# Kernel tuning notes

Measured on AMD Instinct MI355X. Metric: run time of the kernel, lower is better.

Reference implementation:

```python
import jax, jax.numpy as jnp
import numpy as np

B, N, D, H, L, F = 8192, 64, 128, 8, 3, 512
HD = D // H
RADIUS = 3.0
LN_EPS = 1e-5


def _ln(x, g, b):
    m = jnp.mean(x, axis=-1, keepdims=True)
    v = jnp.var(x, axis=-1, keepdims=True)
    return (x - m) / jnp.sqrt(v + LN_EPS) * g + b


def setup_inputs() -> dict:
    key = jax.random.key(0)
    ks = jax.random.split(key, 20)
    def nrm(k, shape, s=0.05):
        return jax.random.normal(k, shape, jnp.float32) * s
    return {
        'ego_context': nrm(ks[0], (B, D), 1.0),
        'ego_pos': nrm(ks[1], (B, 2), 1.0),
        'ego_vel': nrm(ks[2], (B, 2), 1.0),
        'neighbor_pos': nrm(ks[3], (B, N, 2), 1.5),
        'neighbor_vel': nrm(ks[4], (B, N, 2), 1.0),
        'neighbor_mask': jax.random.bernoulli(ks[5], 0.8, (B, N)),
        'np_W': nrm(ks[6], (6, D), 0.3), 'np_b': jnp.zeros((D,), jnp.float32),
        'np_ln_g': jnp.ones((D,), jnp.float32), 'np_ln_b': jnp.zeros((D,), jnp.float32),
        'ego_W': nrm(ks[7], (D, D)), 'ego_b': jnp.zeros((D,), jnp.float32),
        'ego_ln_g': jnp.ones((D,), jnp.float32), 'ego_ln_b': jnp.zeros((D,), jnp.float32),
        'n1_g': jnp.ones((L, D), jnp.float32), 'n1_b': jnp.zeros((L, D), jnp.float32),
        'nkv_g': jnp.ones((L, D), jnp.float32), 'nkv_b': jnp.zeros((L, D), jnp.float32),
        'n2_g': jnp.ones((L, D), jnp.float32), 'n2_b': jnp.zeros((L, D), jnp.float32),
        'Wq': nrm(ks[8], (L, D, D)), 'bq': jnp.zeros((L, D), jnp.float32),
        'Wk': nrm(ks[9], (L, D, D)), 'bk': jnp.zeros((L, D), jnp.float32),
        'Wv': nrm(ks[10], (L, D, D)), 'bv': jnp.zeros((L, D), jnp.float32),
        'Wo': nrm(ks[11], (L, D, D)), 'bo': jnp.zeros((L, D), jnp.float32),
        'W1': nrm(ks[12], (L, D, F)), 'b1': jnp.zeros((L, F), jnp.float32),
        'W2': nrm(ks[13], (L, F, D)), 'b2': jnp.zeros((L, D), jnp.float32),
        'out_W': nrm(ks[14], (D, D)), 'out_b': jnp.zeros((D,), jnp.float32),
        'out_ln_g': jnp.ones((D,), jnp.float32), 'out_ln_b': jnp.zeros((D,), jnp.float32),
    }


def reference(ego_context, ego_pos, ego_vel, neighbor_pos, neighbor_vel, neighbor_mask,
              np_W, np_b, np_ln_g, np_ln_b, ego_W, ego_b, ego_ln_g, ego_ln_b,
              n1_g, n1_b, nkv_g, nkv_b, n2_g, n2_b,
              Wq, bq, Wk, bk, Wv, bv, Wo, bo, W1, b1, W2, b2,
              out_W, out_b, out_ln_g, out_ln_b):
    # relative features (B, N, 6)
    rel_pos = neighbor_pos - ego_pos[:, None, :]
    rel_vel = neighbor_vel - ego_vel[:, None, :]
    dist = jnp.clip(jnp.linalg.norm(rel_pos, axis=-1, keepdims=True), 1e-6, None)
    bearing = jnp.arctan2(rel_pos[..., 1:2] + 1e-8, rel_pos[..., 0:1] + 1e-8)
    rel = jnp.concatenate([rel_pos, rel_vel, dist, bearing], axis=-1)

    # dynamic mask: radius gating + all-masked fixup (mimics key_padding_mask[all_masked,0]=False)
    valid = neighbor_mask & (jnp.linalg.norm(neighbor_pos - ego_pos[:, None, :], axis=-1) < RADIUS)
    all_invalid = ~jnp.any(valid, axis=-1)
    valid = valid | (all_invalid[:, None] & (jnp.arange(N) == 0)[None, :])

    # neighbor_proj: Linear(6,D) -> LN -> ReLU (dropout inactive at eval)
    nb = jax.nn.relu(_ln(rel @ np_W + np_b, np_ln_g, np_ln_b))  # (B, N, D)
    # ego_proj: Linear(D,D) -> LN; keep ego as (B, D) since query length is 1
    x = _ln(ego_context @ ego_W + ego_b, ego_ln_g, ego_ln_b)

    scale = 1.0 / jnp.sqrt(jnp.float32(HD))
    for i in range(L):
        q = _ln(x, n1_g[i], n1_b[i])          # (B, D)
        kv = _ln(nb, nkv_g[i], nkv_b[i])      # (B, N, D)
        Q = (q @ Wq[i] + bq[i]).reshape(B, H, HD)
        K = (kv @ Wk[i] + bk[i]).reshape(B, N, H, HD)
        V = (kv @ Wv[i] + bv[i]).reshape(B, N, H, HD)
        scores = jnp.einsum('bhd,bnhd->bhn', Q, K) * scale
        scores = jnp.where(valid[:, None, :], scores, -1e9)
        attn = jax.nn.softmax(scores, axis=-1)
        ctx = jnp.einsum('bhn,bnhd->bhd', attn, V).reshape(B, D)
        x = x + ctx @ Wo[i] + bo[i]
        y = _ln(x, n2_g[i], n2_b[i])
        x = x + jax.nn.gelu(y @ W1[i] + b1[i], approximate=False) @ W2[i] + b2[i]

    return _ln(x @ out_W + out_b, out_ln_g, out_ln_b)
```

## Files before the change

kernel.cpp:

```cpp
#include <hip/hip_runtime.h>
#include <stdint.h>

typedef unsigned int uint;
typedef unsigned short ushort;
typedef unsigned long long u64;

#define B_   8192
#define D_   128
#define N_   64
#define L_   3

typedef __attribute__((ext_vector_type(8))) short short8;
typedef __attribute__((ext_vector_type(4))) float f32x4;
union FragU { uint4 u; short8 h; };

__device__ __forceinline__ float bf2f(ushort u){ union{uint i; float f;} c; c.i=((uint)u)<<16; return c.f; }
__device__ __forceinline__ float bflo(uint u){ union{uint i; float f;} c; c.i=u<<16; return c.f; }
__device__ __forceinline__ float bfhi(uint u){ union{uint i; float f;} c; c.i=u&0xffff0000u; return c.f; }
__device__ __forceinline__ ushort f2bf(float f){ uint u=__float_as_uint(f); return (ushort)((u + 0x7fffu + ((u>>16)&1u))>>16); }
__device__ __forceinline__ uint pk2(float lo, float hi){ return (uint)f2bf(lo) | (((uint)f2bf(hi))<<16); }
__device__ __forceinline__ float wsum(float v){ for (int o=32;o;o>>=1) v += __shfl_xor(v,o); return v; }

__device__ ushort g_WqT[3*128*128];
__device__ ushort g_WkT[3*128*128];
__device__ ushort g_WvT[3*128*128];
__device__ ushort g_WoT[3*128*128];
__device__ ushort g_W1T[3*512*128];
__device__ ushort g_W2T[3*128*512];
__device__ ushort g_egoT[128*128];
__device__ ushort g_outT[128*128];
__device__ float  g_npRec[128*9];
__device__ ushort g_bqF[384];
__device__ ushort g_bkF[384];
__device__ ushort g_bvF[384];
__device__ ushort g_b1F[1536];
__device__ u64    g_msk[B_];

#define OFF_X   0
#define XSTR    520
#define OFF_XH  8320
#define XHSTR   272
#define OFF_Q   12672
#define QSTR    260
#define OFF_QK  16832
#define QKSTR   272
#define OFF_QB  21184
#define OFF_V   21248
#define OFF_NB  21504
#define NBSTR   272
#define OFF_NT  38912
#define NTSTR   144
#define OFF_AT  57344
#define ATSTR   144
#define OFF_U   59648
#define OFF_CX  61760
#define OFF_H1  21504
#define LDS_SZ  62272

struct P {
  const float *ego, *epos, *evel, *npos, *nvel;
  const int   *mask;
  const float *npW, *npb, *npg, *npbb;
  const float *ego_b, *ego_g, *ego_bb;
  const float *bo, *b2, *out_b, *out_g, *out_bb;
  ushort *nbg;
  float *outp;
};

template<int MODE>
__global__ __launch_bounds__(256,4) void prep_all(P p,
    const float* Wq,const float* bq,const float* n1g,const float* n1b,
    const float* Wk,const float* bk,const float* nkg,const float* nkb,
    const float* Wv,const float* bv,
    const float* W1,const float* b1,const float* n2g,const float* n2b,
    const float* Wo,const float* W2,const float* egoW,const float* outW){
  __shared__ float red[2];
  __shared__ float s_npW[768], s_npP[384];
  __shared__ float s_valid[2][64];
  __shared__ __align__(16) ushort s_T[2][128][68];
  const int bid = blockIdx.x;
  const int tid = threadIdx.x;
  if (bid < 2688){
    int t = tid;
    const float *src,*g,*bb,*bias; ushort *dstW,*dstB; int N;
    if (bid<384){ int l=bid>>7, j=bid&127; src=Wq+l*16384+j; g=n1g+l*128; bb=n1b+l*128; bias=bq+l*128+j; dstW=g_WqT+l*16384+j*128; dstB=g_bqF+l*128+j; N=128; }
    else if (bid<768){ int q=bid-384; int l=q>>7, j=q&127; src=Wk+l*16384+j; g=nkg+l*128; bb=nkb+l*128; bias=bk+l*128+j; dstW=g_WkT+l*16384+j*128; dstB=g_bkF+l*128+j; N=128; }
    else if (bid<1152){ int q=bid-768; int l=q>>7, j=q&127; src=Wv+l*16384+j; g=nkg+l*128; bb=nkb+l*128; bias=bv+l*128+j; dstW=g_WvT+l*16384+j*128; dstB=g_bvF+l*128+j; N=128; }
    else { int q=bid-1152; int l=q/512, j=q%512; src=W1+l*65536+j; g=n2g+l*128; bb=n2b+l*128; bias=b1+l*512+j; dstW=g_W1T+l*65536+j*128; dstB=g_b1F+l*512+j; N=512; }
    if (t<128){
      float wv = src[t*N];
      dstW[t] = f2bf(g[t]*wv);
      float pv = wsum(bb[t]*wv);
      if ((t&63)==0) red[t>>6]=pv;
    }
    __syncthreads();
    if (t==0) *dstB = f2bf(red[0]+red[1]+bias[0]);
  } else if (bid < 3712){
    int pb = bid - 2688, t = tid;
    if (t<128){
      if (pb<384){ int l=pb>>7, j=pb&127; g_WoT[l*16384+j*128+t] = f2bf(Wo[l*16384+t*128+j]); }
      else if (pb<768){ int q=pb-384; int l=q>>7, j=q&127;
        for (int k=t;k<512;k+=128) g_W2T[l*65536+j*512+k] = f2bf(W2[l*65536+k*128+j]); }
      else if (pb<896){ int j=pb-768; g_egoT[j*128+t]=f2bf(egoW[t*128+j]); }
      else { int j=pb-896; g_outT[j*128+t]=f2bf(outW[t*128+j]); }
    }
  } else if (bid == 3712){
    int t = tid;
    if (t<128){
      for (int r=0;r<6;++r) g_npRec[t*9+r]=p.npW[r*128+t];
      g_npRec[t*9+6]=p.npb[t]; g_npRec[t*9+7]=p.npg[t]; g_npRec[t*9+8]=p.npbb[t];
    }
  } else {
    const int bq2 = bid - 3713;
    const int g = tid>>7, t = tid&127;
    const int b = bq2*2+g;
    for (int i=tid;i<768;i+=256) s_npW[i]=p.npW[i];
    if (tid<128){ s_npP[tid]=p.npb[tid]; s_npP[128+tid]=p.npg[tid]; s_npP[256+tid]=p.npbb[tid]; }
    __syncthreads();
    int nn=t>>1, jh=t&1;
    float2 pn = ((const float2*)p.npos)[b*N_+nn];
    float2 vn = ((const float2*)p.nvel)[b*N_+nn];
    float2 pe = ((const float2*)p.epos)[b];
    float2 ve = ((const float2*)p.evel)[b];
    float rx=pn.x-pe.x, ry=pn.y-pe.y, rvx=vn.x-ve.x, rvy=vn.y-ve.y;
    float nrm = sqrtf(rx*rx+ry*ry);
    float dist = fmaxf(nrm,1e-6f), bear = atan2f(ry+1e-8f, rx+1e-8f);
    bool vld = (p.mask[b*N_+nn]!=0) && (nrm<3.0f);
    if (jh==0) s_valid[g][nn] = vld?1.f:0.f;
    float z[64]; float sa=0.f, sb=0.f;
    #pragma unroll
    for (int jj=0;jj<64;++jj){
      int j = jh*64+jj;
      float v = s_npP[j] + rx*s_npW[j] + ry*s_npW[128+j] + rvx*s_npW[256+j]
                         + rvy*s_npW[384+j] + dist*s_npW[512+j] + bear*s_npW[640+j];
      z[jj]=v; sa+=v; sb+=v*v;
    }
    sa += __shfl_xor(sa,1); sb += __shfl_xor(sb,1);
    float m1 = sa*0.0078125f, r1 = rsqrtf(sb*0.0078125f - m1*m1 + 1e-5f);
    float ta=0.f, tb=0.f;
    #pragma unroll
    for (int jj=0;jj<64;++jj){
      int j = jh*64+jj;
      float a = (z[jj]-m1)*r1*s_npP[128+j] + s_npP[256+j];
      a = fmaxf(a,0.f);
      z[jj]=a; ta+=a; tb+=a*a;
    }
    ta += __shfl_xor(ta,1); tb += __shfl_xor(tb,1);
    float m2 = ta*0.0078125f, r2 = rsqrtf(tb*0.0078125f - m2*m2 + 1e-5f);
    uint4* dst4 = (uint4*)((char*)p.nbg + (size_t)b*32768 + (size_t)t*128);
    #pragma unroll
    for (int q8=0;q8<8;++q8){
      uint prs[4];
      #pragma unroll
      for (int qi=0;qi<4;++qi){
        int q = q8*4+qi;
        uint pr = pk2((z[2*q]-m2)*r2, (z[2*q+1]-m2)*r2);
        prs[qi]=pr;
        int d = jh*64 + 2*q;
        s_T[g][d][nn]   = (ushort)pr;
        s_T[g][d+1][nn] = (ushort)(pr>>16);
      }
      uint4 ov; ov.x=prs[0]; ov.y=prs[1]; ov.z=prs[2]; ov.w=prs[3];
      dst4[q8] = ov;
    }
    __syncthreads();
    const int b0 = bq2*2;
    #pragma unroll
    for (int i=0;i<8;++i){
      int idx = tid + i*256;
      int g2 = idx>>10, k = idx&1023;
      int d = k>>3, n0 = (k&7)*8;
      const ushort* srcT = &s_T[g2][d][n0];
      uint2 v0 = *(const uint2*)srcT;
      uint2 v1 = *(const uint2*)(srcT+4);
      uint4 outv; outv.x=v0.x; outv.y=v0.y; outv.z=v1.x; outv.w=v1.y;
      *(uint4*)((char*)p.nbg + (size_t)(b0+g2)*32768 + 16384 + (size_t)k*16) = outv;
    }
    if (tid<2){
      u64 m=0;
      for (int n=0;n<64;++n) if (s_valid[tid][n]>0.5f) m |= (1ULL<<n);
      g_msk[bq2*2+tid] = m;
    }
  }
}

__device__ __forceinline__ void ln_to_xh(char* smem, int tid){
  int b = tid>>4, pp = tid&15;
  const char* xr = smem + OFF_X + b*XSTR + pp*32;
  float v[8];
  #pragma unroll
  for (int i=0;i<4;++i){ float2 t2 = *(const float2*)(xr + i*8); v[2*i]=t2.x; v[2*i+1]=t2.y; }
  float s1=0.f, s2=0.f;
  #pragma unroll
  for (int i=0;i<8;++i){ s1+=v[i]; s2+=v[i]*v[i]; }
  for (int o=1;o<16;o<<=1){ s1 += __shfl_xor(s1,o); s2 += __shfl_xor(s2,o); }
  float m = s1*0.0078125f, rs = rsqrtf(s2*0.0078125f - m*m + 1e-5f);
  uint4 o4;
  o4.x = pk2((v[0]-m)*rs,(v[1]-m)*rs); o4.y = pk2((v[2]-m)*rs,(v[3]-m)*rs);
  o4.z = pk2((v[4]-m)*rs,(v[5]-m)*rs); o4.w = pk2((v[6]-m)*rs,(v[7]-m)*rs);
  *(uint4*)(smem + OFF_XH + b*XHSTR + pp*16) = o4;
}

__device__ __forceinline__ void ln_affine_inplace(char* smem, int tid, const float* g, const float* bb){
  int b = tid>>4, pp = tid&15;
  char* xr = smem + OFF_X + b*XSTR + pp*32;
  float v[8];
  #pragma unroll
  for (int i=0;i<4;++i){ float2 t2 = *(const float2*)(xr + i*8); v[2*i]=t2.x; v[2*i+1]=t2.y; }
  float s1=0.f, s2=0.f;
  #pragma unroll
  for (int i=0;i<8;++i){ s1+=v[i]; s2+=v[i]*v[i]; }
  for (int o=1;o<16;o<<=1){ s1 += __shfl_xor(s1,o); s2 += __shfl_xor(s2,o); }
  float m = s1*0.0078125f, rs = rsqrtf(s2*0.0078125f - m*m + 1e-5f);
  #pragma unroll
  for (int i=0;i<8;++i) v[i] = (v[i]-m)*rs*g[pp*8+i] + bb[pp*8+i];
  #pragma unroll
  for (int i=0;i<4;++i){ float2 t2; t2.x=v[2*i]; t2.y=v[2*i+1]; *(float2*)(xr + i*8) = t2; }
}

__device__ __forceinline__ void cvt_x_to_xh(char* smem, int tid){
  int b = tid>>4, pp = tid&15;
  const char* xr = smem + OFF_X + b*XSTR + pp*32;
  float v[8];
  #pragma unroll
  for (int i=0;i<4;++i){ float2 t2 = *(const float2*)(xr + i*8); v[2*i]=t2.x; v[2*i+1]=t2.y; }
  uint4 o4;
  o4.x=pk2(v[0],v[1]); o4.y=pk2(v[2],v[3]); o4.z=pk2(v[4],v[5]); o4.w=pk2(v[6],v[7]);
  *(uint4*)(smem + OFF_XH + b*XHSTR + pp*16) = o4;
}

__global__ __launch_bounds__(256,2) void st_main3(P p){
  __shared__ __align__(16) char smem[LDS_SZ];
  const int tid = threadIdx.x;
  const int w = tid>>6, l64 = tid&63;
  const int cc = l64&15, qq = l64>>4;
  const int bB = blockIdx.x*16;

  for (int i=tid;i<1088;i+=256) ((uint*)(smem+OFF_QK))[i]=0u;
  if (tid<16) ((float*)(smem+OFF_QB))[tid]=0.f;
  for (int i=tid;i<288;i+=256) ((uint*)(smem+OFF_AT+8*ATSTR))[i]=0u;

  {
    int b_=tid>>4, pp=tid&15;
    const float* src = p.ego + (size_t)(bB+b_)*128 + pp*8;
    float4 v0 = *(const float4*)src, v1 = *(const float4*)(src+4);
    uint4 o4; o4.x=pk2(v0.x,v0.y); o4.y=pk2(v0.z,v0.w); o4.z=pk2(v1.x,v1.y); o4.w=pk2(v1.z,v1.w);
    *(uint4*)(smem + OFF_XH + b_*XHSTR + pp*16) = o4;
  }
  __syncthreads();
  {
    #pragma unroll
    for (int i=0;i<2;++i){
      int nt = w*2+i;
      f32x4 acc = {0.f,0.f,0.f,0.f};
      #pragma unroll
      for (int kt=0;kt<4;++kt){
        FragU a,bF;
        a.u = *(const uint4*)(smem + OFF_XH + cc*XHSTR + kt*64 + qq*16);
        bF.u = *(const uint4*)(g_egoT + (nt*16+cc)*128 + kt*32 + qq*8);
        acc = __builtin_amdgcn_mfma_f32_16x16x32_bf16(a.h, bF.h, acc, 0,0,0);
      }
      int col = nt*16+cc;
      float bv = p.ego_b[col];
      #pragma unroll
      for (int r=0;r<4;++r) *(float*)(smem+OFF_X+(qq*4+r)*XSTR+col*4) = acc[r]+bv;
    }
  }
  __syncthreads();
  ln_affine_inplace(smem, tid, p.ego_g, p.ego_bb);
  __syncthreads();

  for (int li=0; li<L_; ++li){
    ln_to_xh(smem, tid);
    __syncthreads();
    {
      const ushort* W = g_WqT + li*16384;
      #pragma unroll
      for (int i=0;i<2;++i){
        int nt = w*2+i;
        f32x4 acc = {0.f,0.f,0.f,0.f};
        #pragma unroll
        for (int kt=0;kt<4;++kt){
          FragU a,bF;
          a.u = *(const uint4*)(smem + OFF_XH + cc*XHSTR + kt*64 + qq*16);
          bF.u = *(const uint4*)(W + (nt*16+cc)*128 + kt*32 + qq*8);
          acc = __builtin_amdgcn_mfma_f32_16x16x32_bf16(a.h, bF.h, acc, 0,0,0);
        }
        int col = nt*16+cc;
        float bv = bf2f(g_bqF[li*128+col]);
        ushort* Qm = (ushort*)(smem+OFF_Q);
        #pragma unroll
        for (int r=0;r<4;++r) Qm[(qq*4+r)*130 + col] = f2bf(acc[r]+bv);
      }
    }
    __syncthreads();

    for (int bl=0; bl<16; ++bl){
      const int b = bB + bl;
      const char* nbg_b = (const char*)p.nbg + (size_t)b*32768;

      const int sn = w*16 + (l64>>2), seg = l64&3;
      const int dt = tid>>1, hf = tid&1;
      uint4 nbr[4], ntr[4];
      #pragma unroll
      for (int i=0;i<4;++i) nbr[i] = *(const uint4*)(nbg_b + sn*256 + (seg+4*i)*16);
      #pragma unroll
      for (int i=0;i<4;++i) ntr[i] = *(const uint4*)(nbg_b + 16384 + dt*128 + hf*64 + i*16);

      {
        int h = (w<<1) + (l64>>5);
        int d4 = (l64&31)*4;
        const ushort* Wk = g_WkT + li*16384;
        float a0=0.f,a1=0.f,a2=0.f,a3=0.f, qb=0.f;
        #pragma unroll
        for (int j=0;j<16;++j){
          float qv = bf2f(*(const ushort*)(smem + OFF_Q + bl*QSTR + (h*16+j)*2));
          uint2 wv = *(const uint2*)(Wk + (h*16+j)*128 + d4);
          a0 += qv*bflo(wv.x); a1 += qv*bfhi(wv.x);
          a2 += qv*bflo(wv.y); a3 += qv*bfhi(wv.y);
          qb += qv * bf2f(g_bkF[li*128 + h*16 + j]);
        }
        uint2 o; o.x = pk2(a0,a1); o.y = pk2(a2,a3);
        *(uint2*)(smem + OFF_QK + h*QKSTR + d4*2) = o;
        if ((l64&31)==0) *(float*)(smem+OFF_QB + h*4) = qb;
      }

      #pragma unroll
      for (int i=0;i<4;++i) *(uint4*)(smem + OFF_NB + sn*NBSTR + (seg+4*i)*16) = nbr[i];
      #pragma unroll
      for (int i=0;i<4;++i) *(uint4*)(smem + OFF_NT + dt*NTSTR + hf*64 + i*16) = ntr[i];
      __syncthreads();

      {
        FragU bfr[4];
        #pragma unroll
        for (int kt=0;kt<4;++kt) bfr[kt].u = *(const uint4*)(smem + OFF_QK + cc*QKSTR + kt*64 + qq*16);
        f32x4 c[4];
        #pragma unroll
        for (int mt=0;mt<4;++mt){
          f32x4 acc = {0.f,0.f,0.f,0.f};
          #pragma unroll
          for (int kt=0;kt<4;++kt){
            FragU a; a.u = *(const uint4*)(smem + OFF_NB + (mt*16+cc)*NBSTR + kt*64 + qq*16);
            acc = __builtin_amdgcn_mfma_f32_16x16x32_bf16(a.h, bfr[kt].h, acc, 0,0,0);
          }
          c[mt]=acc;
        }
        u64 mv = g_msk[b];
        bool none = (mv==0ULL);
        float qbv = *(const float*)(smem+OFF_QB+cc*4);
        float sc[16];
        #pragma unroll
        for (int mt=0;mt<4;++mt)
          #pragma unroll
          for (int r=0;r<4;++r){
            int k = mt*4+r; int n = mt*16+qq*4+r;
            bool ok = (((mv>>n)&1ULL)!=0ULL) || (none && n==0);
            sc[k] = ok ? 0.25f*(c[mt][r]+qbv) : -1e9f;
          }
        float mx=-3e38f;
        #pragma unroll
        for (int k=0;k<16;++k) mx=fmaxf(mx,sc[k]);
        mx = fmaxf(mx,__shfl_xor(mx,16)); mx = fmaxf(mx,__shfl_xor(mx,32));
        float ex[16]; float se=0.f;
        #pragma unroll
        for (int k=0;k<16;++k){ ex[k]=__expf(sc[k]-mx); se+=ex[k]; }
        se += __shfl_xor(se,16); se += __shfl_xor(se,32);
        float inv = 1.f/se;
        if (w==0 && cc<8){
          ushort* A = (ushort*)(smem+OFF_AT);
          #pragma unroll
          for (int mt=0;mt<4;++mt)
            #pragma unroll
            for (int r=0;r<4;++r) A[cc*72 + (mt*16+qq*4+r)] = f2bf(ex[mt*4+r]*inv);
        }
      }
      __syncthreads();

      {
        #pragma unroll
        for (int i=0;i<2;++i){
          int nt = w*2 + i;
          f32x4 acc={0.f,0.f,0.f,0.f};
          #pragma unroll
          for (int kt=0;kt<2;++kt){
            FragU a,bF;
            a.u = *(const uint4*)(smem + OFF_AT + cc*ATSTR + kt*64 + qq*16);
            bF.u = *(const uint4*)(smem + OFF_NT + (nt*16+cc)*NTSTR + kt*64 + qq*16);
            acc = __builtin_amdgcn_mfma_f32_16x16x32_bf16(a.h, bF.h, acc, 0,0,0);
          }
          if (qq<2){
            ushort* U = (ushort*)(smem+OFF_U);
            #pragma unroll
            for (int r=0;r<4;++r) U[(qq*4+r)*132 + nt*16+cc] = f2bf(acc[r]);
          }
        }
      }
      __syncthreads();

      {
        int jj = l64>>1, dh = l64&1;
        int j = w*32 + jj;
        int h = j>>4;
        const ushort* Wv = g_WvT + li*16384 + j*128;
        float acc = (dh==0) ? bf2f(g_bvF[li*128+j]) : 0.f;
        #pragma unroll
        for (int i8=0;i8<8;++i8){
          int d = dh*64 + i8*8;
          uint2 u0 = *(const uint2*)(smem + OFF_U + h*264 + d*2);
          uint2 u1 = *(const uint2*)(smem + OFF_U + h*264 + d*2 + 8);
          uint4 wv = *(const uint4*)(Wv + d);
          acc += bflo(u0.x)*bflo(wv.x) + bfhi(u0.x)*bfhi(wv.x);
          acc += bflo(u0.y)*bflo(wv.y) + bfhi(u0.y)*bfhi(wv.y);
          acc += bflo(u1.x)*bflo(wv.z) + bfhi(u1.x)*bfhi(wv.z);
          acc += bflo(u1.y)*bflo(wv.w) + bfhi(u1.y)*bfhi(wv.w);
        }
        acc += __shfl_xor(acc,1);
        if (dh==0) *(float*)(smem+OFF_CX + j*4) = acc;
      }
      __syncthreads();

      {
        int jj = l64>>1, dh = l64&1;
        int j = w*32 + jj;
        const ushort* Wo = g_WoT + li*16384 + j*128;
        float acc = (dh==0) ? p.bo[li*128+j] : 0.f;
        #pragma unroll
        for (int i8=0;i8<8;++i8){
          int d = dh*64 + i8*8;
          float4 c0 = *(const float4*)(smem + OFF_CX + d*4);
          float4 c1 = *(const float4*)(smem + OFF_CX + d*4 + 16);
          uint4 wv = *(const uint4*)(Wo + d);
          acc += c0.x*bflo(wv.x) + c0.y*bfhi(wv.x) + c0.z*bflo(wv.y) + c0.w*bfhi(wv.y);
          acc += c1.x*bflo(wv.z) + c1.y*bfhi(wv.z) + c1.z*bflo(wv.w) + c1.w*bfhi(wv.w);
        }
        acc += __shfl_xor(acc,1);
        if (dh==0){
          float* xp = (float*)(smem + OFF_X + bl*XSTR + j*4);
          *xp += acc;
        }
      }
      __syncthreads();
    }

    ln_to_xh(smem, tid);
    __syncthreads();
    {
      FragU afr[4];
      #pragma unroll
      for (int kt=0;kt<4;++kt) afr[kt].u = *(const uint4*)(smem+OFF_XH + cc*XHSTR + kt*64 + qq*16);
      const ushort* W = g_W1T + li*65536;
      ushort* H = (ushort*)(smem+OFF_H1);
      #pragma unroll
      for (int i=0;i<8;++i){
        int nt = w*8+i;
        f32x4 acc={0.f,0.f,0.f,0.f};
        #pragma unroll
        for (int kt=0;kt<4;++kt){
          FragU bF; bF.u = *(const uint4*)(W + (nt*16+cc)*128 + kt*32 + qq*8);
          acc = __builtin_amdgcn_mfma_f32_16x16x32_bf16(afr[kt].h, bF.h, acc, 0,0,0);
        }
        int col = nt*16+cc;
        float bv = bf2f(g_b1F[li*512+col]);
        #pragma unroll
        for (int r=0;r<4;++r){
          float v = acc[r]+bv;
          v = 0.5f*v*(1.f+erff(v*0.70710678118654752f));
          H[(qq*4+r)*520 + col] = f2bf(v);
        }
      }
    }
    __syncthreads();
    {
      const ushort* W = g_W2T + li*65536;
      #pragma unroll
      for (int i=0;i<2;++i){
        int nt = w*2+i;
        f32x4 acc={0.f,0.f,0.f,0.f};
        #pragma unroll
        for (int kt=0;kt<16;++kt){
          FragU a,bF;
          a.u = *(const uint4*)(smem+OFF_H1 + cc*1040 + kt*64 + qq*16);
          bF.u = *(const uint4*)(W + (nt*16+cc)*512 + kt*32 + qq*8);
          acc = __builtin_amdgcn_mfma_f32_16x16x32_bf16(a.h, bF.h, acc, 0,0,0);
        }
        int col = nt*16+cc;
        float bv = p.b2[li*128+col];
        #pragma unroll
        for (int r=0;r<4;++r){
          float* xp = (float*)(smem+OFF_X+(qq*4+r)*XSTR+col*4);
          *xp += acc[r]+bv;
        }
      }
    }
    __syncthreads();
  }

  cvt_x_to_xh(smem, tid);
  __syncthreads();
  {
    #pragma unroll
    for (int i=0;i<2;++i){
      int nt = w*2+i;
      f32x4 acc = {0.f,0.f,0.f,0.f};
      #pragma unroll
      for (int kt=0;kt<4;++kt){
        FragU a,bF;
        a.u = *(const uint4*)(smem + OFF_XH + cc*XHSTR + kt*64 + qq*16);
        bF.u = *(const uint4*)(g_outT + (nt*16+cc)*128 + kt*32 + qq*8);
        acc = __builtin_amdgcn_mfma_f32_16x16x32_bf16(a.h, bF.h, acc, 0,0,0);
      }
      int col = nt*16+cc;
      float bv = p.out_b[col];
      #pragma unroll
      for (int r=0;r<4;++r) *(float*)(smem+OFF_X+(qq*4+r)*XSTR+col*4) = acc[r]+bv;
    }
  }
  __syncthreads();
  {
    int b_=tid>>4, pp=tid&15;
    const char* xr = smem + OFF_X + b_*XSTR + pp*32;
    float v[8];
    #pragma unroll
    for (int i=0;i<4;++i){ float2 t2 = *(const float2*)(xr + i*8); v[2*i]=t2.x; v[2*i+1]=t2.y; }
    float s1=0.f, s2=0.f;
    #pragma unroll
    for (int i=0;i<8;++i){ s1+=v[i]; s2+=v[i]*v[i]; }
    for (int o=1;o<16;o<<=1){ s1 += __shfl_xor(s1,o); s2 += __shfl_xor(s2,o); }
    float m = s1*0.0078125f, rs = rsqrtf(s2*0.0078125f - m*m + 1e-5f);
    float4 o0,o1;
    o0.x=(v[0]-m)*rs*p.out_g[pp*8+0]+p.out_bb[pp*8+0];
    o0.y=(v[1]-m)*rs*p.out_g[pp*8+1]+p.out_bb[pp*8+1];
    o0.z=(v[2]-m)*rs*p.out_g[pp*8+2]+p.out_bb[pp*8+2];
    o0.w=(v[3]-m)*rs*p.out_g[pp*8+3]+p.out_bb[pp*8+3];
    o1.x=(v[4]-m)*rs*p.out_g[pp*8+4]+p.out_bb[pp*8+4];
    o1.y=(v[5]-m)*rs*p.out_g[pp*8+5]+p.out_bb[pp*8+5];
    o1.z=(v[6]-m)*rs*p.out_g[pp*8+6]+p.out_bb[pp*8+6];
    o1.w=(v[7]-m)*rs*p.out_g[pp*8+7]+p.out_bb[pp*8+7];
    float* dst = p.outp + (size_t)(bB+b_)*128 + pp*8;
    *(float4*)dst = o0; *(float4*)(dst+4) = o1;
  }
}

__global__ __launch_bounds__(256,2) void st_main0(P p){
  __shared__ __align__(16) char smem[LDS_SZ];
  const int tid = threadIdx.x;
  const int w = tid>>6, l64 = tid&63;
  const int cc = l64&15, qq = l64>>4;
  const int bB = blockIdx.x*16;

  for (int i=tid;i<1088;i+=256) ((uint*)(smem+OFF_QK))[i]=0u;
  if (tid<16) ((float*)(smem+OFF_QB))[tid]=0.f;
  for (int i=tid;i<288;i+=256) ((uint*)(smem+OFF_AT+8*ATSTR))[i]=0u;

  {
    int b_=tid>>4, pp=tid&15;
    const float* src = p.ego + (size_t)(bB+b_)*128 + pp*8;
    float4 v0 = *(const float4*)src, v1 = *(const float4*)(src+4);
    uint4 o4; o4.x=pk2(v0.x,v0.y); o4.y=pk2(v0.z,v0.w); o4.z=pk2(v1.x,v1.y); o4.w=pk2(v1.z,v1.w);
    *(uint4*)(smem + OFF_XH + b_*XHSTR + pp*16) = o4;
  }
  __syncthreads();
  {
    #pragma unroll
    for (int i=0;i<2;++i){
      int nt = w*2+i;
      f32x4 acc = {0.f,0.f,0.f,0.f};
      #pragma unroll
      for (int kt=0;kt<4;++kt){
        FragU a,bF;
        a.u = *(const uint4*)(smem + OFF_XH + cc*XHSTR + kt*64 + qq*16);
        bF.u = *(const uint4*)(g_egoT + (nt*16+cc)*128 + kt*32 + qq*8);
        acc = __builtin_amdgcn_mfma_f32_16x16x32_bf16(a.h, bF.h, acc, 0,0,0);
      }
      int col = nt*16+cc;
      float bv = p.ego_b[col];
      #pragma unroll
      for (int r=0;r<4;++r) *(float*)(smem+OFF_X+(qq*4+r)*XSTR+col*4) = acc[r]+bv;
    }
  }
  __syncthreads();
  ln_affine_inplace(smem, tid, p.ego_g, p.ego_bb);
  __syncthreads();

  for (int li=0; li<L_; ++li){
    ln_to_xh(smem, tid);
    __syncthreads();
    {
      const ushort* W = g_WqT + li*16384;
      #pragma unroll
      for (int i=0;i<2;++i){
        int nt = w*2+i;
        f32x4 acc = {0.f,0.f,0.f,0.f};
        #pragma unroll
        for (int kt=0;kt<4;++kt){
          FragU a,bF;
          a.u = *(const uint4*)(smem + OFF_XH + cc*XHSTR + kt*64 + qq*16);
          bF.u = *(const uint4*)(W + (nt*16+cc)*128 + kt*32 + qq*8);
          acc = __builtin_amdgcn_mfma_f32_16x16x32_bf16(a.h, bF.h, acc, 0,0,0);
        }
        int col = nt*16+cc;
        float bv = bf2f(g_bqF[li*128+col]);
        ushort* Qm = (ushort*)(smem+OFF_Q);
        #pragma unroll
        for (int r=0;r<4;++r) Qm[(qq*4+r)*130 + col] = f2bf(acc[r]+bv);
      }
    }
    __syncthreads();

    for (int bl=0; bl<16; ++bl){
      const int b = bB + bl;
      {
        int n = w*16 + (l64>>2), jq = l64&3;
        float2 pn = ((const float2*)p.npos)[b*N_+n];
        float2 vn = ((const float2*)p.nvel)[b*N_+n];
        float2 pe = ((const float2*)p.epos)[b];
        float2 ve = ((const float2*)p.evel)[b];
        float rx=pn.x-pe.x, ry=pn.y-pe.y, rvx=vn.x-ve.x, rvy=vn.y-ve.y;
        float nrm = sqrtf(rx*rx+ry*ry);
        float dist = fmaxf(nrm,1e-6f), bear = atan2f(ry+1e-8f, rx+1e-8f);
        if (jq==0){
          bool vld = (p.mask[b*N_+n]!=0) && (nrm<3.0f);
          *(float*)(smem+OFF_V+n*4) = vld?1.f:0.f;
        }
        float z[32]; float sa=0.f, sb=0.f;
        #pragma unroll
        for (int jj=0;jj<32;++jj){
          const float* rec = g_npRec + (jq*32+jj)*9;
          float4 r0 = *(const float4*)rec;
          float4 r1 = *(const float4*)(rec+4);
          float v = r1.z + rx*r0.x + ry*r0.y + rvx*r0.z + rvy*r0.w + dist*r1.x + bear*r1.y;
          z[jj]=v; sa+=v; sb+=v*v;
        }
        sa += __shfl_xor(sa,1); sb += __shfl_xor(sb,1);
        sa += __shfl_xor(sa,2); sb += __shfl_xor(sb,2);
        float m1 = sa*0.0078125f, r1s = rsqrtf(sb*0.0078125f - m1*m1 + 1e-5f);
        float ta=0.f, tb=0.f;
        #pragma unroll
        for (int jj=0;jj<32;++jj){
          const float* rec = g_npRec + (jq*32+jj)*9;
          float a = (z[jj]-m1)*r1s*rec[7] + rec[8];
          a = fmaxf(a,0.f);
          z[jj]=a; ta+=a; tb+=a*a;
        }
        ta += __shfl_xor(ta,1); tb += __shfl_xor(tb,1);
        ta += __shfl_xor(ta,2); tb += __shfl_xor(tb,2);
        float m2 = ta*0.0078125f, r2s = rsqrtf(tb*0.0078125f - m2*m2 + 1e-5f);
        ushort* T = (ushort*)(smem+OFF_NT);
        #pragma unroll
        for (int q2=0;q2<16;++q2){
          uint pr = pk2((z[2*q2]-m2)*r2s, (z[2*q2+1]-m2)*r2s);
          *(uint*)(smem + OFF_NB + n*NBSTR + jq*64 + q2*4) = pr;
          int d = jq*32 + q2*2;
          T[d*72 + n] = (ushort)pr;
          T[(d+1)*72 + n] = (ushort)(pr>>16);
        }
      }
      {
        int h = (w<<1) + (l64>>5);
        int d4 = (l64&31)*4;
        const ushort* Wk = g_WkT + li*16384;
        float a0=0.f,a1=0.f,a2=0.f,a3=0.f, qb=0.f;
        #pragma unroll
        for (int j=0;j<16;++j){
          float qv = bf2f(*(const ushort*)(smem + OFF_Q + bl*QSTR + (h*16+j)*2));
          uint2 wv = *(const uint2*)(Wk + (h*16+j)*128 + d4);
          a0 += qv*bflo(wv.x); a1 += qv*bfhi(wv.x);
          a2 += qv*bflo(wv.y); a3 += qv*bfhi(wv.y);
          qb += qv * bf2f(g_bkF[li*128 + h*16 + j]);
        }
        uint2 o; o.x = pk2(a0,a1); o.y = pk2(a2,a3);
        *(uint2*)(smem + OFF_QK + h*QKSTR + d4*2) = o;
        if ((l64&31)==0) *(float*)(smem+OFF_QB + h*4) = qb;
      }
      __syncthreads();

      {
        FragU bfr[4];
        #pragma unroll
        for (int kt=0;kt<4;++kt) bfr[kt].u = *(const uint4*)(smem + OFF_QK + cc*QKSTR + kt*64 + qq*16);
        f32x4 c[4];
        #pragma unroll
        for (int mt=0;mt<4;++mt){
          f32x4 acc = {0.f,0.f,0.f,0.f};
          #pragma unroll
          for (int kt=0;kt<4;++kt){
            FragU a; a.u = *(const uint4*)(smem + OFF_NB + (mt*16+cc)*NBSTR + kt*64 + qq*16);
            acc = __builtin_amdgcn_mfma_f32_16x16x32_bf16(a.h, bfr[kt].h, acc, 0,0,0);
          }
          c[mt]=acc;
        }
        float qbv = *(const float*)(smem+OFF_QB+cc*4);
        float fl[16]; float anyv=0.f;
        #pragma unroll
        for (int mt=0;mt<4;++mt)
          #pragma unroll
          for (int r=0;r<4;++r){
            int n = mt*16 + qq*4 + r;
            float f = *(const float*)(smem+OFF_V+n*4);
            fl[mt*4+r]=f; anyv+=f;
          }
        bool none = (__ballot(anyv>0.5f)==0ULL);
        float sc[16];
        #pragma unroll
        for (int mt=0;mt<4;++mt)
          #pragma unroll
          for (int r=0;r<4;++r){
            int k = mt*4+r; int n = mt*16+qq*4+r;
            bool ok = (fl[k]>0.5f) || (none && n==0);
            sc[k] = ok ? 0.25f*(c[mt][r]+qbv) : -1e9f;
          }
        float mx=-3e38f;
        #pragma unroll
        for (int k=0;k<16;++k) mx=fmaxf(mx,sc[k]);
        mx = fmaxf(mx,__shfl_xor(mx,16)); mx = fmaxf(mx,__shfl_xor(mx,32));
        float ex[16]; float se=0.f;
        #pragma unroll
        for (int k=0;k<16;++k){ ex[k]=__expf(sc[k]-mx); se+=ex[k]; }
        se += __shfl_xor(se,16); se += __shfl_xor(se,32);
        float inv = 1.f/se;
        if (w==0 && cc<8){
          ushort* A = (ushort*)(smem+OFF_AT);
          #pragma unroll
          for (int mt=0;mt<4;++mt)
            #pragma unroll
            for (int r=0;r<4;++r) A[cc*72 + (mt*16+qq*4+r)] = f2bf(ex[mt*4+r]*inv);
        }
      }
      __syncthreads();

      {
        #pragma unroll
        for (int i=0;i<2;++i){
          int nt = w*2 + i;
          f32x4 acc={0.f,0.f,0.f,0.f};
          #pragma unroll
          for (int kt=0;kt<2;++kt){
            FragU a,bF;
            a.u = *(const uint4*)(smem + OFF_AT + cc*ATSTR + kt*64 + qq*16);
            bF.u = *(const uint4*)(smem + OFF_NT + (nt*16+cc)*NTSTR + kt*64 + qq*16);
            acc = __builtin_amdgcn_mfma_f32_16x16x32_bf16(a.h, bF.h, acc, 0,0,0);
          }
          if (qq<2){
            ushort* U = (ushort*)(smem+OFF_U);
            #pragma unroll
            for (int r=0;r<4;++r) U[(qq*4+r)*132 + nt*16+cc] = f2bf(acc[r]);
          }
        }
      }
      __syncthreads();

      {
        int jj = l64>>1, dh = l64&1;
        int j = w*32 + jj;
        int h = j>>4;
        const ushort* Wv = g_WvT + li*16384 + j*128;
        float acc = (dh==0) ? bf2f(g_bvF[li*128+j]) : 0.f;
        #pragma unroll
        for (int i8=0;i8<8;++i8){
          int d = dh*64 + i8*8;
          uint2 u0 = *(const uint2*)(smem + OFF_U + h*264 + d*2);
          uint2 u1 = *(const uint2*)(smem + OFF_U + h*264 + d*2 + 8);
          uint4 wv = *(const uint4*)(Wv + d);
          acc += bflo(u0.x)*bflo(wv.x) + bfhi(u0.x)*bfhi(wv.x);
          acc += bflo(u0.y)*bflo(wv.y) + bfhi(u0.y)*bfhi(wv.y);
          acc += bflo(u1.x)*bflo(wv.z) + bfhi(u1.x)*bfhi(wv.z);
          acc += bflo(u1.y)*bflo(wv.w) + bfhi(u1.y)*bfhi(wv.w);
        }
        acc += __shfl_xor(acc,1);
        if (dh==0) *(float*)(smem+OFF_CX + j*4) = acc;
      }
      __syncthreads();

      {
        int jj = l64>>1, dh = l64&1;
        int j = w*32 + jj;
        const ushort* Wo = g_WoT + li*16384 + j*128;
        float acc = (dh==0) ? p.bo[li*128+j] : 0.f;
        #pragma unroll
        for (int i8=0;i8<8;++i8){
          int d = dh*64 + i8*8;
          float4 c0 = *(const float4*)(smem + OFF_CX + d*4);
          float4 c1 = *(const float4*)(smem + OFF_CX + d*4 + 16);
          uint4 wv = *(const uint4*)(Wo + d);
          acc += c0.x*bflo(wv.x) + c0.y*bfhi(wv.x) + c0.z*bflo(wv.y) + c0.w*bfhi(wv.y);
          acc += c1.x*bflo(wv.z) + c1.y*bfhi(wv.z) + c1.z*bflo(wv.w) + c1.w*bfhi(wv.w);
        }
        acc += __shfl_xor(acc,1);
        if (dh==0){
          float* xp = (float*)(smem + OFF_X + bl*XSTR + j*4);
          *xp += acc;
        }
      }
      __syncthreads();
    }

    ln_to_xh(smem, tid);
    __syncthreads();
    {
      FragU afr[4];
      #pragma unroll
      for (int kt=0;kt<4;++kt) afr[kt].u = *(const uint4*)(smem+OFF_XH + cc*XHSTR + kt*64 + qq*16);
      const ushort* W = g_W1T + li*65536;
      ushort* H = (ushort*)(smem+OFF_H1);
      #pragma unroll
      for (int i=0;i<8;++i){
        int nt = w*8+i;
        f32x4 acc={0.f,0.f,0.f,0.f};
        #pragma unroll
        for (int kt=0;kt<4;++kt){
          FragU bF; bF.u = *(const uint4*)(W + (nt*16+cc)*128 + kt*32 + qq*8);
          acc = __builtin_amdgcn_mfma_f32_16x16x32_bf16(afr[kt].h, bF.h, acc, 0,0,0);
        }
        int col = nt*16+cc;
        float bv = bf2f(g_b1F[li*512+col]);
        #pragma unroll
        for (int r=0;r<4;++r){
          float v = acc[r]+bv;
          v = 0.5f*v*(1.f+erff(v*0.70710678118654752f));
          H[(qq*4+r)*520 + col] = f2bf(v);
        }
      }
    }
    __syncthreads();
    {
      const ushort* W = g_W2T + li*65536;
      #pragma unroll
      for (int i=0;i<2;++i){
        int nt = w*2+i;
        f32x4 acc={0.f,0.f,0.f,0.f};
        #pragma unroll
        for (int kt=0;kt<16;++kt){
          FragU a,bF;
          a.u = *(const uint4*)(smem+OFF_H1 + cc*1040 + kt*64 + qq*16);
          bF.u = *(const uint4*)(W + (nt*16+cc)*512 + kt*32 + qq*8);
          acc = __builtin_amdgcn_mfma_f32_16x16x32_bf16(a.h, bF.h, acc, 0,0,0);
        }
        int col = nt*16+cc;
        float bv = p.b2[li*128+col];
        #pragma unroll
        for (int r=0;r<4;++r){
          float* xp = (float*)(smem+OFF_X+(qq*4+r)*XSTR+col*4);
          *xp += acc[r]+bv;
        }
      }
    }
    __syncthreads();
  }

  cvt_x_to_xh(smem, tid);
  __syncthreads();
  {
    #pragma unroll
    for (int i=0;i<2;++i){
      int nt = w*2+i;
      f32x4 acc = {0.f,0.f,0.f,0.f};
      #pragma unroll
      for (int kt=0;kt<4;++kt){
        FragU a,bF;
        a.u = *(const uint4*)(smem + OFF_XH + cc*XHSTR + kt*64 + qq*16);
        bF.u = *(const uint4*)(g_outT + (nt*16+cc)*128 + kt*32 + qq*8);
        acc = __builtin_amdgcn_mfma_f32_16x16x32_bf16(a.h, bF.h, acc, 0,0,0);
      }
      int col = nt*16+cc;
      float bv = p.out_b[col];
      #pragma unroll
      for (int r=0;r<4;++r) *(float*)(smem+OFF_X+(qq*4+r)*XSTR+col*4) = acc[r]+bv;
    }
  }
  __syncthreads();
  {
    int b_=tid>>4, pp=tid&15;
    const char* xr = smem + OFF_X + b_*XSTR + pp*32;
    float v[8];
    #pragma unroll
    for (int i=0;i<4;++i){ float2 t2 = *(const float2*)(xr + i*8); v[2*i]=t2.x; v[2*i+1]=t2.y; }
    float s1=0.f, s2=0.f;
    #pragma unroll
    for (int i=0;i<8;++i){ s1+=v[i]; s2+=v[i]*v[i]; }
    for (int o=1;o<16;o<<=1){ s1 += __shfl_xor(s1,o); s2 += __shfl_xor(s2,o); }
    float m = s1*0.0078125f, rs = rsqrtf(s2*0.0078125f - m*m + 1e-5f);
    float4 o0,o1;
    o0.x=(v[0]-m)*rs*p.out_g[pp*8+0]+p.out_bb[pp*8+0];
    o0.y=(v[1]-m)*rs*p.out_g[pp*8+1]+p.out_bb[pp*8+1];
    o0.z=(v[2]-m)*rs*p.out_g[pp*8+2]+p.out_bb[pp*8+2];
    o0.w=(v[3]-m)*rs*p.out_g[pp*8+3]+p.out_bb[pp*8+3];
    o1.x=(v[4]-m)*rs*p.out_g[pp*8+4]+p.out_bb[pp*8+4];
    o1.y=(v[5]-m)*rs*p.out_g[pp*8+5]+p.out_bb[pp*8+5];
    o1.z=(v[6]-m)*rs*p.out_g[pp*8+6]+p.out_bb[pp*8+6];
    o1.w=(v[7]-m)*rs*p.out_g[pp*8+7]+p.out_bb[pp*8+7];
    float* dst = p.outp + (size_t)(bB+b_)*128 + pp*8;
    *(float4*)dst = o0; *(float4*)(dst+4) = o1;
  }
}

extern "C" void kernel_launch(void* const* d_in, const int* in_sizes, int n_in,
                              void* d_out, int out_size, void* d_ws, size_t ws_size,
                              hipStream_t stream){
  (void)in_sizes; (void)n_in; (void)out_size;
  char* ws = (char*)d_ws;
  const size_t NEED2 = (size_t)B_*32768;

  P p;
  p.ego=(const float*)d_in[0]; p.epos=(const float*)d_in[1]; p.evel=(const float*)d_in[2];
  p.npos=(const float*)d_in[3]; p.nvel=(const float*)d_in[4]; p.mask=(const int*)d_in[5];
  p.npW=(const float*)d_in[6]; p.npb=(const float*)d_in[7]; p.npg=(const float*)d_in[8]; p.npbb=(const float*)d_in[9];
  p.ego_b=(const float*)d_in[11]; p.ego_g=(const float*)d_in[12]; p.ego_bb=(const float*)d_in[13];
  p.bo=(const float*)d_in[27]; p.b2=(const float*)d_in[31];
  p.out_b=(const float*)d_in[33]; p.out_g=(const float*)d_in[34]; p.out_bb=(const float*)d_in[35];
  p.nbg = (ushort*)ws;
  p.outp=(float*)d_out;

  #define PREP_ARGS p, \
      (const float*)d_in[20],(const float*)d_in[21],(const float*)d_in[14],(const float*)d_in[15], \
      (const float*)d_in[22],(const float*)d_in[23],(const float*)d_in[16],(const float*)d_in[17], \
      (const float*)d_in[24],(const float*)d_in[25], \
      (const float*)d_in[28],(const float*)d_in[29],(const float*)d_in[18],(const float*)d_in[19], \
      (const float*)d_in[26],(const float*)d_in[30],(const float*)d_in[10],(const float*)d_in[32]

  if (ws_size >= NEED2){
    prep_all<1><<<3713 + B_/2, 256, 0, stream>>>(PREP_ARGS);
    st_main3<<<B_/16,256,0,stream>>>(p);
  } else {
    prep_all<0><<<3713, 256, 0, stream>>>(PREP_ARGS);
    st_main0<<<B_/16,256,0,stream>>>(p);
  }
  #undef PREP_ARGS
}
```

Before: 753.8 us.

## Store neighbor features once and transpose in LDS inside main kernel

```diff
diff --git a/kernel.cpp b/kernel.cpp
--- a/kernel.cpp
+++ b/kernel.cpp
@@ -77,7 +77,6 @@
   __shared__ float red[2];
   __shared__ float s_npW[768], s_npP[384];
   __shared__ float s_valid[2][64];
-  __shared__ __align__(16) ushort s_T[2][128][68];
   const int bid = blockIdx.x;
   const int tid = threadIdx.x;
   if (bid < 2688){
@@ -147,35 +146,19 @@
     }
     ta += __shfl_xor(ta,1); tb += __shfl_xor(tb,1);
     float m2 = ta*0.0078125f, r2 = rsqrtf(tb*0.0078125f - m2*m2 + 1e-5f);
-    uint4* dst4 = (uint4*)((char*)p.nbg + (size_t)b*32768 + (size_t)t*128);
+    uint4* dst4 = (uint4*)((char*)p.nbg + (size_t)b*16384 + (size_t)t*128);
     #pragma unroll
     for (int q8=0;q8<8;++q8){
       uint prs[4];
       #pragma unroll
       for (int qi=0;qi<4;++qi){
         int q = q8*4+qi;
-        uint pr = pk2((z[2*q]-m2)*r2, (z[2*q+1]-m2)*r2);
-        prs[qi]=pr;
-        int d = jh*64 + 2*q;
-        s_T[g][d][nn]   = (ushort)pr;
-        s_T[g][d+1][nn] = (ushort)(pr>>16);
+        prs[qi] = pk2((z[2*q]-m2)*r2, (z[2*q+1]-m2)*r2);
       }
       uint4 ov; ov.x=prs[0]; ov.y=prs[1]; ov.z=prs[2]; ov.w=prs[3];
       dst4[q8] = ov;
     }
     __syncthreads();
-    const int b0 = bq2*2;
-    #pragma unroll
-    for (int i=0;i<8;++i){
-      int idx = tid + i*256;
-      int g2 = idx>>10, k = idx&1023;
-      int d = k>>3, n0 = (k&7)*8;
-      const ushort* srcT = &s_T[g2][d][n0];
-      uint2 v0 = *(const uint2*)srcT;
-      uint2 v1 = *(const uint2*)(srcT+4);
-      uint4 outv; outv.x=v0.x; outv.y=v0.y; outv.z=v1.x; outv.w=v1.y;
-      *(uint4*)((char*)p.nbg + (size_t)(b0+g2)*32768 + 16384 + (size_t)k*16) = outv;
-    }
     if (tid<2){
       u64 m=0;
       for (int n=0;n<64;++n) if (s_valid[tid][n]>0.5f) m |= (1ULL<<n);
@@ -229,7 +212,7 @@
   *(uint4*)(smem + OFF_XH + b*XHSTR + pp*16) = o4;
 }
 
-__global__ __launch_bounds__(256,2) void st_main3(P p){
+__global__ __launch_bounds__(256,2) void st_main5(P p){
   __shared__ __align__(16) char smem[LDS_SZ];
   const int tid = threadIdx.x;
   const int w = tid>>6, l64 = tid&63;
@@ -297,16 +280,26 @@
 
     for (int bl=0; bl<16; ++bl){
       const int b = bB + bl;
-      const char* nbg_b = (const char*)p.nbg + (size_t)b*32768;
-
-      const int sn = w*16 + (l64>>2), seg = l64&3;
-      const int dt = tid>>1, hf = tid&1;
-      uint4 nbr[4], ntr[4];
-      #pragma unroll
-      for (int i=0;i<4;++i) nbr[i] = *(const uint4*)(nbg_b + sn*256 + (seg+4*i)*16);
-      #pragma unroll
-      for (int i=0;i<4;++i) ntr[i] = *(const uint4*)(nbg_b + 16384 + dt*128 + hf*64 + i*16);
-
+      {
+        int n = w*16 + (l64>>2), seg = l64&3;
+        if (seg==0){
+          u64 mv = g_msk[b];
+          *(float*)(smem+OFF_V+n*4) = ((mv>>n)&1ULL) ? 1.f : 0.f;
+        }
+        const uint4* src = (const uint4*)(p.nbg + (size_t)b*8192 + n*128);
+        ushort* T = (ushort*)(smem+OFF_NT);
+        #pragma unroll
+        for (int i=0;i<4;++i){
+          int ci = seg + i*4;
+          uint4 v = src[ci];
+          *(uint4*)(smem + OFF_NB + n*NBSTR + ci*16) = v;
+          int d0 = ci*8;
+          T[(d0+0)*72+n]=(ushort)v.x; T[(d0+1)*72+n]=(ushort)(v.x>>16);
+          T[(d0+2)*72+n]=(ushort)v.y; T[(d0+3)*72+n]=(ushort)(v.y>>16);
+          T[(d0+4)*72+n]=(ushort)v.z; T[(d0+5)*72+n]=(ushort)(v.z>>16);
+          T[(d0+6)*72+n]=(ushort)v.w; T[(d0+7)*72+n]=(ushort)(v.w>>16);
+        }
+      }
       {
         int h = (w<<1) + (l64>>5);
         int d4 = (l64&31)*4;
@@ -324,11 +317,6 @@
         *(uint2*)(smem + OFF_QK + h*QKSTR + d4*2) = o;
         if ((l64&31)==0) *(float*)(smem+OFF_QB + h*4) = qb;
       }
-
-      #pragma unroll
-      for (int i=0;i<4;++i) *(uint4*)(smem + OFF_NB + sn*NBSTR + (seg+4*i)*16) = nbr[i];
-      #pragma unroll
-      for (int i=0;i<4;++i) *(uint4*)(smem + OFF_NT + dt*NTSTR + hf*64 + i*16) = ntr[i];
       __syncthreads();
 
       {
@@ -346,16 +334,24 @@
           }
           c[mt]=acc;
         }
-        u64 mv = g_msk[b];
-        bool none = (mv==0ULL);
         float qbv = *(const float*)(smem+OFF_QB+cc*4);
+        float fl[16]; float anyv=0.f;
+        #pragma unroll
+        for (int mt=0;mt<4;++mt)
+          #pragma unroll
+          for (int r=0;r<4;++r){
+            int n = mt*16 + qq*4 + r;
+            float f = *(const float*)(smem+OFF_V+n*4);
+            fl[mt*4+r]=f; anyv+=f;
+          }
+        bool none = (__ballot(anyv>0.5f)==0ULL);
         float sc[16];
         #pragma unroll
         for (int mt=0;mt<4;++mt)
           #pragma unroll
           for (int r=0;r<4;++r){
             int k = mt*4+r; int n = mt*16+qq*4+r;
-            bool ok = (((mv>>n)&1ULL)!=0ULL) || (none && n==0);
+            bool ok = (fl[k]>0.5f) || (none && n==0);
             sc[k] = ok ? 0.25f*(c[mt][r]+qbv) : -1e9f;
           }
         float mx=-3e38f;
@@ -899,7 +895,7 @@
                               hipStream_t stream){
   (void)in_sizes; (void)n_in; (void)out_size;
   char* ws = (char*)d_ws;
-  const size_t NEED2 = (size_t)B_*32768;
+  const size_t NEED1 = (size_t)B_*16384;
 
   P p;
   p.ego=(const float*)d_in[0]; p.epos=(const float*)d_in[1]; p.evel=(const float*)d_in[2];
@@ -918,9 +914,9 @@
       (const float*)d_in[28],(const float*)d_in[29],(const float*)d_in[18],(const float*)d_in[19], \
       (const float*)d_in[26],(const float*)d_in[30],(const float*)d_in[10],(const float*)d_in[32]
 
-  if (ws_size >= NEED2){
+  if (ws_size >= NEED1){
     prep_all<1><<<3713 + B_/2, 256, 0, stream>>>(PREP_ARGS);
-    st_main3<<<B_/16,256,0,stream>>>(p);
+    st_main5<<<B_/16,256,0,stream>>>(p);
   } else {
     prep_all<0><<<3713, 256, 0, stream>>>(PREP_ARGS);
     st_main0<<<B_/16,256,0,stream>>>(p);
```

Result: faster. 629.9 us (-16.4%).
